# Kernel optimization log

Measured on AMD Instinct MI355X. Metric: run time of the kernel, lower is better.

## Reference

```python
import jax, jax.numpy as jnp
import numpy as np

N_NODES = 50000


def gcn_norm(edge_index, edge_weight, n):
    """PyG GCNConv normalization: add self-loops (weight 1), sym-normalize."""
    src, dst = edge_index[0], edge_index[1]
    loop = jnp.arange(n, dtype=src.dtype)
    src = jnp.concatenate([src, loop])
    dst = jnp.concatenate([dst, loop])
    w = jnp.concatenate([edge_weight, jnp.ones((n,), dtype=edge_weight.dtype)])
    deg = jax.ops.segment_sum(w, dst, num_segments=n)  # in-degree w/ self-loops
    dis = jnp.where(deg > 0, jax.lax.rsqrt(deg), 0.0)  # deg^{-1/2}, inf -> 0
    norm = dis[src] * w * dis[dst]                      # [E+N]
    return src, dst, norm


def gcn_conv(x, src, dst, norm, W, b):
    h = x @ W                                            # [N, F_out]
    msg = norm[:, None] * h[src]                         # gather + scale
    out = jax.ops.segment_sum(msg, dst, num_segments=x.shape[0])  # scatter-add
    return out + b


def setup_inputs() -> dict:
    key = jax.random.key(0)
    ks = jax.random.split(key, 10)
    n, e = N_NODES, 800000
    in_dim, hidden, out_dim = 256, 128, 64
    x = jax.random.normal(ks[0], (n, in_dim), dtype=jnp.float32)
    edge_index = jax.random.randint(ks[1], (2, e), 0, n, dtype=jnp.int32)
    edge_weight = jax.random.uniform(ks[2], (e,), dtype=jnp.float32)
    def glorot(k, fi, fo):
        lim = float(np.sqrt(6.0 / (fi + fo)))
        return jax.random.uniform(k, (fi, fo), minval=-lim, maxval=lim, dtype=jnp.float32)
    return {
        "x": x, "edge_index": edge_index, "edge_weight": edge_weight,
        "W1": glorot(ks[3], in_dim, hidden), "b1": jnp.zeros((hidden,), jnp.float32),
        "W2": glorot(ks[4], hidden, hidden), "b2": jnp.zeros((hidden,), jnp.float32),
        "W3": glorot(ks[5], hidden, out_dim), "b3": jnp.zeros((out_dim,), jnp.float32),
    }


def reference(x, edge_index, edge_weight, W1, b1, W2, b2, W3, b3):
    n = x.shape[0]
    src, dst, norm = gcn_norm(edge_index, edge_weight, n)  # cached=True: shared
    h = jax.nn.relu(gcn_conv(x, src, dst, norm, W1, b1))   # dropout: eval mode no-op
    h = jax.nn.relu(gcn_conv(h, src, dst, norm, W2, b2))
    h = gcn_conv(h, src, dst, norm, W3, b3)
    return h
```

## Files before the change

kernel.cpp:

```cpp
#include <hip/hip_runtime.h>
#include <hip/hip_bf16.h>
#include <stdint.h>

#define NODES 50000
#define EDGES 800000

#define EPB 4096
#define NBLK ((EDGES + EPB - 1) / EPB)
#define NBUK ((NODES + 63) / 64)
#define NBUKP 1024
#define CAP 2560

#define NTILE (NODES / 16)

typedef short bf16x8 __attribute__((ext_vector_type(8)));
typedef float f32x4 __attribute__((ext_vector_type(4)));

__device__ __forceinline__ unsigned short f2bf(float f) {
    union { float f; unsigned u; } v; v.f = f;
    unsigned r = v.u + 0x7fff + ((v.u >> 16) & 1);
    return (unsigned short)(r >> 16);
}
__device__ __forceinline__ float bf2f(unsigned short h) {
    union { float f; unsigned u; } v; v.u = ((unsigned)h) << 16;
    return v.f;
}
__device__ __forceinline__ float bflo(unsigned hv) {
    union { float f; unsigned u; } v; v.u = hv << 16;
    return v.f;
}
__device__ __forceinline__ float bfhi(unsigned hv) {
    union { float f; unsigned u; } v; v.u = hv & 0xffff0000u;
    return v.f;
}

__device__ __forceinline__ void wfrag_one(const float* __restrict__ W, unsigned short* Wf,
                                          int idx, int K, int Nn) {
    int NT = Nn >> 4;
    int lane = idx & 63;
    int f = idx >> 6;
    int nt = f % NT;
    int k0 = (f / NT) << 5;
    int n = (nt << 4) + (lane & 15);
    int kk = k0 + ((lane >> 4) << 3);
    unsigned short o[8];
#pragma unroll
    for (int j = 0; j < 8; j++) o[j] = f2bf(W[(kk + j) * Nn + n]);
    ((uint4*)Wf)[idx] = *(uint4*)o;
}

__global__ void k_setup_hist(const int* __restrict__ dst, unsigned* __restrict__ hist,
                             int* __restrict__ cursor,
                             const float* __restrict__ W1, unsigned short* Wf1,
                             const float* __restrict__ W2, unsigned short* Wf2,
                             const float* __restrict__ W3, unsigned short* Wf3) {
    if ((int)blockIdx.x < NBLK) {
        __shared__ unsigned cnt[NBUK];
        int t = threadIdx.x;
        for (int i = t; i < NBUK; i += 256) cnt[i] = 0;
        __syncthreads();
        int base = blockIdx.x * EPB;
#pragma unroll
        for (int i = 0; i < EPB / 256; i++) {
            int e = base + i * 256 + t;
            if (e < EDGES) atomicAdd(&cnt[((unsigned)dst[e]) >> 6], 1u);
        }
        __syncthreads();
        for (int b = t; b < NBUK; b += 256) hist[b * NBLK + blockIdx.x] = cnt[b];
    } else {
        int idx = (blockIdx.x - NBLK) * 256 + threadIdx.x;
        if (idx == 0) *cursor = 0;
        if (idx < 4096) wfrag_one(W1, Wf1, idx, 256, 128);
        else if (idx < 6144) wfrag_one(W2, Wf2, idx - 4096, 128, 128);
        else if (idx < 7168) wfrag_one(W3, Wf3, idx - 6144, 128, 64);
    }
}

__global__ void k_hscan(unsigned* __restrict__ hist, int2* __restrict__ brange,
                        int* __restrict__ cursor) {
    __shared__ int sm[256];
    __shared__ int s_base;
    int b = blockIdx.x, t = threadIdx.x;
    int v = (t < NBLK) ? (int)hist[b * NBLK + t] : 0;
    sm[t] = v;
    __syncthreads();
    for (int off = 1; off < 256; off <<= 1) {
        int x2 = (t >= off) ? sm[t - off] : 0;
        __syncthreads();
        sm[t] += x2;
        __syncthreads();
    }
    int total = sm[255];
    if (t == 0) s_base = atomicAdd(cursor, total);
    __syncthreads();
    if (t < NBLK) hist[b * NBLK + t] = (unsigned)(s_base + sm[t] - v);
    if (t == 0) { int2 r; r.x = s_base; r.y = total; brange[b] = r; }
}

template <int K, int Nn, bool A_F32>
__device__ __forceinline__ void gemm_tile(const void* __restrict__ A_,
                                          const uint4* __restrict__ Wf,
                                          unsigned short* __restrict__ Hout, int tile) {
    constexpr int NT = Nn / 16;
    int lane = threadIdx.x & 63;
    if (tile * 16 >= NODES) return;
    int row = tile * 16 + (lane & 15);
    int kbase = (lane >> 4) * 8;

    f32x4 acc[NT];
#pragma unroll
    for (int i = 0; i < NT; i++) acc[i] = (f32x4){0.f, 0.f, 0.f, 0.f};

    for (int k0 = 0; k0 < K; k0 += 32) {
        bf16x8 a;
        if (A_F32) {
            const float* A = (const float*)A_;
            const float4* pp = (const float4*)&A[(size_t)row * K + k0 + kbase];
            float4 u0 = pp[0], u1 = pp[1];
            unsigned short t[8];
            t[0] = f2bf(u0.x); t[1] = f2bf(u0.y); t[2] = f2bf(u0.z); t[3] = f2bf(u0.w);
            t[4] = f2bf(u1.x); t[5] = f2bf(u1.y); t[6] = f2bf(u1.z); t[7] = f2bf(u1.w);
            a = *(bf16x8*)t;
        } else {
            const unsigned short* A = (const unsigned short*)A_;
            a = *(const bf16x8*)&A[(size_t)row * K + k0 + kbase];
        }
        int fbase = (k0 >> 5) * NT;
#pragma unroll
        for (int nt = 0; nt < NT; nt++) {
            uint4 braw = Wf[(fbase + nt) * 64 + lane];
            bf16x8 b = *(bf16x8*)&braw;
            acc[nt] = __builtin_amdgcn_mfma_f32_16x16x32_bf16(b, a, acc[nt], 0, 0, 0);
        }
    }
    int xr = lane & 15;
    int wg = lane >> 4;
#pragma unroll
    for (int nt = 0; nt < NT; nt++) {
        uint2 pk;
        pk.x = (unsigned)f2bf(acc[nt][0]) | ((unsigned)f2bf(acc[nt][1]) << 16);
        pk.y = (unsigned)f2bf(acc[nt][2]) | ((unsigned)f2bf(acc[nt][3]) << 16);
        ((uint2*)Hout)[(((size_t)(tile * 16 + xr) * Nn + nt * 16) >> 2) + wg] = pk;
    }
}

__global__ __launch_bounds__(1024) void
k_sort_gemm1(const int* __restrict__ src, const int* __restrict__ dst,
             const float* __restrict__ w, const unsigned* __restrict__ gbase,
             int2* __restrict__ rec,
             const float* __restrict__ x, const uint4* __restrict__ Wf1,
             unsigned short* __restrict__ h) {
    __shared__ unsigned long long rec_lds[EPB];
    __shared__ unsigned cnt[NBUKP];
    __shared__ unsigned lst[NBUKP];
    __shared__ unsigned gb[NBUK];
    __shared__ int sm[1024];

    int blk = blockIdx.x;
    int t = threadIdx.x;
    if (blk & 1) {
        gemm_tile<256, 128, true>((const void*)x, Wf1, h, (blk >> 1) * 16 + (t >> 6));
        return;
    }
    int sb = blk >> 1;
    if (t < NBUK) gb[t] = gbase[t * NBLK + sb];
    cnt[t] = 0;
    __syncthreads();

    int base = sb * EPB;
    int nrec = EDGES - base; if (nrec > EPB) nrec = EPB;

#pragma unroll
    for (int i = 0; i < EPB / 1024; i++) {
        int e = base + i * 1024 + t;
        if (e < EDGES) atomicAdd(&cnt[((unsigned)dst[e]) >> 6], 1u);
    }
    __syncthreads();

    int v = (int)cnt[t];
    sm[t] = v;
    __syncthreads();
    for (int off = 1; off < 1024; off <<= 1) {
        int x2 = (t >= off) ? sm[t - off] : 0;
        __syncthreads();
        sm[t] += x2;
        __syncthreads();
    }
    lst[t] = (unsigned)(sm[t] - v);
    cnt[t] = 0;
    __syncthreads();

#pragma unroll
    for (int i = 0; i < EPB / 1024; i++) {
        int e = base + i * 1024 + t;
        if (e < EDGES) {
            unsigned d = (unsigned)dst[e];
            unsigned b = d >> 6;
            unsigned r = atomicAdd(&cnt[b], 1u);
            unsigned meta = (unsigned)src[e] | ((d & 63u) << 16) | (b << 22);
            rec_lds[lst[b] + r] = (unsigned long long)meta |
                                  ((unsigned long long)__float_as_uint(w[e]) << 32);
        }
    }
    __syncthreads();

    for (int i = t; i < nrec; i += 1024) {
        unsigned long long vv = rec_lds[i];
        unsigned meta = (unsigned)vv;
        unsigned b = meta >> 22;
        unsigned gpos = gb[b] + ((unsigned)i - lst[b]);
        int2 rc; rc.x = (int)(meta & 0x3FFFFFu); rc.y = (int)(vv >> 32);
        rec[gpos] = rc;
    }
}

__global__ void k_sub(int2* __restrict__ rec, const int2* __restrict__ brange,
                      float* __restrict__ dis, int2* __restrict__ rsc) {
    __shared__ int2 stage[CAP];
    __shared__ unsigned short ipos[CAP];
    __shared__ unsigned cnt[64];
    __shared__ unsigned lst[64];
    __shared__ float degw[64];
    int t = threadIdx.x, b = blockIdx.x;
    int2 br = brange[b];
    int base = br.x;
    int n = br.y; if (n > CAP) n = CAP;

    if (t < 64) { cnt[t] = 0; degw[t] = 0.f; }
    __syncthreads();
    for (int i = t; i < n; i += 256) {
        int2 rc = rec[base + i];
        stage[i] = rc;
        unsigned dl = ((unsigned)rc.x >> 16) & 63u;
        atomicAdd(&cnt[dl], 1u);
        atomicAdd(&degw[dl], __int_as_float(rc.y));
    }
    __syncthreads();
    if (t == 0) {
        unsigned run = 0;
        for (int j = 0; j < 64; j++) { lst[j] = run; run += cnt[j]; }
    }
    __syncthreads();
    if (t < 64) {
        int node = b * 64 + t;
        if (node < NODES) {
            dis[node] = rsqrtf(1.0f + degw[t]);
            int2 rs; rs.x = base + (int)lst[t]; rs.y = (int)cnt[t];
            rsc[node] = rs;
        }
    }
    if (t < 64) cnt[t] = 0;
    __syncthreads();
    for (int i = t; i < n; i += 256) {
        unsigned dl = ((unsigned)stage[i].x >> 16) & 63u;
        unsigned r = atomicAdd(&cnt[dl], 1u);
        ipos[lst[dl] + r] = (unsigned short)i;
    }
    __syncthreads();
    for (int i = t; i < n; i += 256) {
        rec[base + i] = stage[ipos[i]];
    }
}

template <int K, int Nn, bool A_F32>
__global__ void k_gemm(const void* __restrict__ A_, const uint4* __restrict__ Wf,
                       unsigned short* __restrict__ Hout) {
    gemm_tile<K, Nn, A_F32>(A_, Wf, Hout, blockIdx.x * 4 + (threadIdx.x >> 6));
}

template <int F, bool RELU, bool OUT_F32>
__global__ void k_agg(const unsigned short* __restrict__ H, const int2* __restrict__ rec,
                      const int2* __restrict__ rsc, const float* __restrict__ dis,
                      const float* __restrict__ bias, void* __restrict__ out_) {
    constexpr int VPT = F / 64;
    int lane = threadIdx.x & 63;
    int node = blockIdx.x * 4 + (threadIdx.x >> 6);
    if (node >= NODES) return;
    node = __builtin_amdgcn_readfirstlane(node);

    const unsigned* H32 = (const unsigned*)H;

    float dn = dis[node];
    float acc0, acc1 = 0.f;
    if (VPT == 2) {
        unsigned hv = H32[node * 64 + lane];
        acc0 = dn * bflo(hv);
        acc1 = dn * bfhi(hv);
    } else {
        acc0 = dn * bf2f(H[node * 64 + lane]);
    }

    int2 rs = rsc[node];
    int beg = rs.x, end = rs.x + rs.y;
    int last = end - 1;
    for (int j = beg; j < end; j += 8) {
        int ss[8]; float nn[8];
#pragma unroll
        for (int q = 0; q < 8; q++) {
            int idx = j + q;
            idx = (idx < last) ? idx : last;
            int2 rc = rec[idx];
            ss[q] = rc.x & 0xFFFF;
            nn[q] = (j + q < end) ? __int_as_float(rc.y) : 0.0f;
        }
#pragma unroll
        for (int q = 0; q < 8; q++) nn[q] *= dis[ss[q]];
        if (VPT == 2) {
            unsigned hh[8];
#pragma unroll
            for (int q = 0; q < 8; q++) hh[q] = H32[ss[q] * 64 + lane];
#pragma unroll
            for (int q = 0; q < 8; q++) {
                acc0 += nn[q] * bflo(hh[q]);
                acc1 += nn[q] * bfhi(hh[q]);
            }
        } else {
            unsigned short hh[8];
#pragma unroll
            for (int q = 0; q < 8; q++) hh[q] = H[ss[q] * 64 + lane];
#pragma unroll
            for (int q = 0; q < 8; q++) acc0 += nn[q] * bf2f(hh[q]);
        }
    }

    if (OUT_F32) {
        float* out = (float*)out_;
        if (VPT == 2) {
            float x0 = dn * acc0 + bias[lane * 2];
            float x1 = dn * acc1 + bias[lane * 2 + 1];
            if (RELU) { x0 = fmaxf(x0, 0.f); x1 = fmaxf(x1, 0.f); }
            out[(size_t)node * F + lane * 2] = x0;
            out[(size_t)node * F + lane * 2 + 1] = x1;
        } else {
            float x0 = dn * acc0 + bias[lane];
            if (RELU) x0 = fmaxf(x0, 0.f);
            out[(size_t)node * F + lane] = x0;
        }
    } else {
        unsigned short* out = (unsigned short*)out_;
        if (VPT == 2) {
            float x0 = dn * acc0 + bias[lane * 2];
            float x1 = dn * acc1 + bias[lane * 2 + 1];
            if (RELU) { x0 = fmaxf(x0, 0.f); x1 = fmaxf(x1, 0.f); }
            unsigned pk = (unsigned)f2bf(x0) | ((unsigned)f2bf(x1) << 16);
            *(unsigned*)&out[(size_t)node * F + lane * 2] = pk;
        } else {
            float x0 = dn * acc0 + bias[lane];
            if (RELU) x0 = fmaxf(x0, 0.f);
            out[(size_t)node * F + lane] = f2bf(x0);
        }
    }
}


extern "C" void kernel_launch(void* const* d_in, const int* in_sizes, int n_in,
                              void* d_out, int out_size, void* d_ws, size_t ws_size,
                              hipStream_t stream) {
    const float* x  = (const float*)d_in[0];
    const int*   ei = (const int*)d_in[1];
    const float* w  = (const float*)d_in[2];
    const float* W1 = (const float*)d_in[3];
    const float* b1 = (const float*)d_in[4];
    const float* W2 = (const float*)d_in[5];
    const float* b2 = (const float*)d_in[6];
    const float* W3 = (const float*)d_in[7];
    const float* b3 = (const float*)d_in[8];
    const int* src = ei;
    const int* dst = ei + EDGES;

    char* p = (char*)d_ws;
    auto alloc = [&](size_t n) { char* r = p; p += (n + 511) & ~(size_t)511; return r; };
    unsigned*       hist   = (unsigned*)alloc((size_t)NBUK * NBLK * 4);
    int2*           brange = (int2*)alloc((size_t)NBUK * 8);
    int*            cursor = (int*)alloc(4);
    int2*           rec    = (int2*)alloc((size_t)EDGES * 8);
    float*          dis    = (float*)alloc(NODES * 4);
    int2*           rsc    = (int2*)alloc((size_t)NODES * 8);
    unsigned short* h      = (unsigned short*)alloc((size_t)NODES * 128 * 2);
    unsigned short* xb     = (unsigned short*)alloc((size_t)NODES * 128 * 2);
    unsigned short* wf1    = (unsigned short*)alloc(256 * 128 * 2);
    unsigned short* wf2    = (unsigned short*)alloc(128 * 128 * 2);
    unsigned short* wf3    = (unsigned short*)alloc(128 * 64 * 2);

    const int TB = 256;

    hipLaunchKernelGGL(k_setup_hist, dim3(NBLK + 28), dim3(TB), 0, stream,
                       dst, hist, cursor, W1, wf1, W2, wf2, W3, wf3);
    hipLaunchKernelGGL(k_hscan, dim3(NBUK), dim3(TB), 0, stream, hist, brange, cursor);
    hipLaunchKernelGGL(k_sort_gemm1, dim3(2 * NBLK), dim3(1024), 0, stream,
                       src, dst, w, hist, rec, x, (const uint4*)wf1, h);
    hipLaunchKernelGGL(k_sub, dim3(NBUK), dim3(TB), 0, stream, rec, brange, dis, rsc);

    int nb_gemm = (NTILE + 3) / 4;
    int nb_agg  = (NODES + 3) / 4;

    hipLaunchKernelGGL((k_agg<128, true, false>), dim3(nb_agg), dim3(TB), 0, stream, h, rec, rsc, dis, b1, (void*)xb);

    hipLaunchKernelGGL((k_gemm<128, 128, false>), dim3(nb_gemm), dim3(TB), 0, stream, (const void*)xb, (const uint4*)wf2, h);
    hipLaunchKernelGGL((k_agg<128, true, false>), dim3(nb_agg), dim3(TB), 0, stream, h, rec, rsc, dis, b2, (void*)xb);

    hipLaunchKernelGGL((k_gemm<128, 64, false>), dim3(nb_gemm), dim3(TB), 0, stream, (const void*)xb, (const uint4*)wf3, h);
    hipLaunchKernelGGL((k_agg<64, false, true>), dim3(nb_agg), dim3(TB), 0, stream, h, rec, rsc, dis, b3, d_out);
}
```

Measured before the change: 305.7 us.

## Split sort from layer-1 GEMM and reuse scanned histogram counts in sort

```diff
diff --git a/kernel.cpp b/kernel.cpp
--- a/kernel.cpp
+++ b/kernel.cpp
@@ -76,8 +76,8 @@
     }
 }
 
-__global__ void k_hscan(unsigned* __restrict__ hist, int2* __restrict__ brange,
-                        int* __restrict__ cursor) {
+__global__ void k_hscan(const unsigned* __restrict__ hist, uint2* __restrict__ cbB,
+                        int2* __restrict__ brange, int* __restrict__ cursor) {
     __shared__ int sm[256];
     __shared__ int s_base;
     int b = blockIdx.x, t = threadIdx.x;
@@ -93,8 +93,128 @@
     int total = sm[255];
     if (t == 0) s_base = atomicAdd(cursor, total);
     __syncthreads();
-    if (t < NBLK) hist[b * NBLK + t] = (unsigned)(s_base + sm[t] - v);
+    if (t < NBLK) {
+        uint2 cb; cb.x = (unsigned)v; cb.y = (unsigned)(s_base + sm[t] - v);
+        cbB[(size_t)t * NBUKP + b] = cb;
+    }
     if (t == 0) { int2 r; r.x = s_base; r.y = total; brange[b] = r; }
+}
+
+__global__ __launch_bounds__(1024) void
+k_sort(const int* __restrict__ src, const int* __restrict__ dst,
+       const float* __restrict__ w, const uint2* __restrict__ cbB,
+       int2* __restrict__ rec) {
+    __shared__ unsigned long long rec_lds[EPB];
+    __shared__ unsigned cnt[NBUKP];
+    __shared__ unsigned lst[NBUKP];
+    __shared__ unsigned gb[NBUKP];
+    __shared__ int wsum[16];
+
+    int sb = blockIdx.x;
+    int t = threadIdx.x;
+    int lane = t & 63;
+    int wid = t >> 6;
+
+    uint2 cb = cbB[(size_t)sb * NBUKP + t];
+    int v = (t < NBUK) ? (int)cb.x : 0;
+    gb[t] = (t < NBUK) ? cb.y : 0u;
+
+    int incl = v;
+#pragma unroll
+    for (int d = 1; d < 64; d <<= 1) {
+        int y = __shfl_up(incl, d, 64);
+        if (lane >= d) incl += y;
+    }
+    if (lane == 63) wsum[wid] = incl;
+    __syncthreads();
+    if (wid == 0) {
+        int s = (lane < 16) ? wsum[lane] : 0;
+#pragma unroll
+        for (int d = 1; d < 16; d <<= 1) {
+            int y = __shfl_up(s, d, 16);
+            if ((lane & 15) >= d) s += y;
+        }
+        if (lane < 16) wsum[lane] = s;
+    }
+    cnt[t] = 0;
+    __syncthreads();
+    int wpre = (wid > 0) ? wsum[wid - 1] : 0;
+    lst[t] = (unsigned)(wpre + incl - v);
+    __syncthreads();
+
+    int base = sb * EPB;
+    int nrec = EDGES - base; if (nrec > EPB) nrec = EPB;
+
+#pragma unroll
+    for (int i = 0; i < EPB / 1024; i++) {
+        int e = base + i * 1024 + t;
+        if (e < EDGES) {
+            unsigned d = (unsigned)dst[e];
+            unsigned b = d >> 6;
+            unsigned r = atomicAdd(&cnt[b], 1u);
+            unsigned meta = (unsigned)src[e] | ((d & 63u) << 16) | (b << 22);
+            rec_lds[lst[b] + r] = (unsigned long long)meta |
+                                  ((unsigned long long)__float_as_uint(w[e]) << 32);
+        }
+    }
+    __syncthreads();
+
+    for (int i = t; i < nrec; i += 1024) {
+        unsigned long long vv = rec_lds[i];
+        unsigned meta = (unsigned)vv;
+        unsigned b = meta >> 22;
+        unsigned gpos = gb[b] + ((unsigned)i - lst[b]);
+        int2 rc; rc.x = (int)(meta & 0x3FFFFFu); rc.y = (int)(vv >> 32);
+        rec[gpos] = rc;
+    }
+}
+
+__global__ void k_sub(int2* __restrict__ rec, const int2* __restrict__ brange,
+                      float* __restrict__ dis, int2* __restrict__ rsc) {
+    __shared__ int2 stage[CAP];
+    __shared__ unsigned short ipos[CAP];
+    __shared__ unsigned cnt[64];
+    __shared__ unsigned lst[64];
+    __shared__ float degw[64];
+    int t = threadIdx.x, b = blockIdx.x;
+    int2 br = brange[b];
+    int base = br.x;
+    int n = br.y; if (n > CAP) n = CAP;
+
+    if (t < 64) { cnt[t] = 0; degw[t] = 0.f; }
+    __syncthreads();
+    for (int i = t; i < n; i += 256) {
+        int2 rc = rec[base + i];
+        stage[i] = rc;
+        unsigned dl = ((unsigned)rc.x >> 16) & 63u;
+        atomicAdd(&cnt[dl], 1u);
+        atomicAdd(&degw[dl], __int_as_float(rc.y));
+    }
+    __syncthreads();
+    if (t == 0) {
+        unsigned run = 0;
+        for (int j = 0; j < 64; j++) { lst[j] = run; run += cnt[j]; }
+    }
+    __syncthreads();
+    if (t < 64) {
+        int node = b * 64 + t;
+        if (node < NODES) {
+            dis[node] = rsqrtf(1.0f + degw[t]);
+            int2 rs; rs.x = base + (int)lst[t]; rs.y = (int)cnt[t];
+            rsc[node] = rs;
+        }
+    }
+    if (t < 64) cnt[t] = 0;
+    __syncthreads();
+    for (int i = t; i < n; i += 256) {
+        unsigned dl = ((unsigned)stage[i].x >> 16) & 63u;
+        unsigned r = atomicAdd(&cnt[dl], 1u);
+        ipos[lst[dl] + r] = (unsigned short)i;
+    }
+    __syncthreads();
+    for (int i = t; i < n; i += 256) {
+        rec[base + i] = stage[ipos[i]];
+    }
 }
 
 template <int K, int Nn, bool A_F32>
@@ -141,124 +261,6 @@
         pk.x = (unsigned)f2bf(acc[nt][0]) | ((unsigned)f2bf(acc[nt][1]) << 16);
         pk.y = (unsigned)f2bf(acc[nt][2]) | ((unsigned)f2bf(acc[nt][3]) << 16);
         ((uint2*)Hout)[(((size_t)(tile * 16 + xr) * Nn + nt * 16) >> 2) + wg] = pk;
-    }
-}
-
-__global__ __launch_bounds__(1024) void
-k_sort_gemm1(const int* __restrict__ src, const int* __restrict__ dst,
-             const float* __restrict__ w, const unsigned* __restrict__ gbase,
-             int2* __restrict__ rec,
-             const float* __restrict__ x, const uint4* __restrict__ Wf1,
-             unsigned short* __restrict__ h) {
-    __shared__ unsigned long long rec_lds[EPB];
-    __shared__ unsigned cnt[NBUKP];
-    __shared__ unsigned lst[NBUKP];
-    __shared__ unsigned gb[NBUK];
-    __shared__ int sm[1024];
-
-    int blk = blockIdx.x;
-    int t = threadIdx.x;
-    if (blk & 1) {
-        gemm_tile<256, 128, true>((const void*)x, Wf1, h, (blk >> 1) * 16 + (t >> 6));
-        return;
-    }
-    int sb = blk >> 1;
-    if (t < NBUK) gb[t] = gbase[t * NBLK + sb];
-    cnt[t] = 0;
-    __syncthreads();
-
-    int base = sb * EPB;
-    int nrec = EDGES - base; if (nrec > EPB) nrec = EPB;
-
-#pragma unroll
-    for (int i = 0; i < EPB / 1024; i++) {
-        int e = base + i * 1024 + t;
-        if (e < EDGES) atomicAdd(&cnt[((unsigned)dst[e]) >> 6], 1u);
-    }
-    __syncthreads();
-
-    int v = (int)cnt[t];
-    sm[t] = v;
-    __syncthreads();
-    for (int off = 1; off < 1024; off <<= 1) {
-        int x2 = (t >= off) ? sm[t - off] : 0;
-        __syncthreads();
-        sm[t] += x2;
-        __syncthreads();
-    }
-    lst[t] = (unsigned)(sm[t] - v);
-    cnt[t] = 0;
-    __syncthreads();
-
-#pragma unroll
-    for (int i = 0; i < EPB / 1024; i++) {
-        int e = base + i * 1024 + t;
-        if (e < EDGES) {
-            unsigned d = (unsigned)dst[e];
-            unsigned b = d >> 6;
-            unsigned r = atomicAdd(&cnt[b], 1u);
-            unsigned meta = (unsigned)src[e] | ((d & 63u) << 16) | (b << 22);
-            rec_lds[lst[b] + r] = (unsigned long long)meta |
-                                  ((unsigned long long)__float_as_uint(w[e]) << 32);
-        }
-    }
-    __syncthreads();
-
-    for (int i = t; i < nrec; i += 1024) {
-        unsigned long long vv = rec_lds[i];
-        unsigned meta = (unsigned)vv;
-        unsigned b = meta >> 22;
-        unsigned gpos = gb[b] + ((unsigned)i - lst[b]);
-        int2 rc; rc.x = (int)(meta & 0x3FFFFFu); rc.y = (int)(vv >> 32);
-        rec[gpos] = rc;
-    }
-}
-
-__global__ void k_sub(int2* __restrict__ rec, const int2* __restrict__ brange,
-                      float* __restrict__ dis, int2* __restrict__ rsc) {
-    __shared__ int2 stage[CAP];
-    __shared__ unsigned short ipos[CAP];
-    __shared__ unsigned cnt[64];
-    __shared__ unsigned lst[64];
-    __shared__ float degw[64];
-    int t = threadIdx.x, b = blockIdx.x;
-    int2 br = brange[b];
-    int base = br.x;
-    int n = br.y; if (n > CAP) n = CAP;
-
-    if (t < 64) { cnt[t] = 0; degw[t] = 0.f; }
-    __syncthreads();
-    for (int i = t; i < n; i += 256) {
-        int2 rc = rec[base + i];
-        stage[i] = rc;
-        unsigned dl = ((unsigned)rc.x >> 16) & 63u;
-        atomicAdd(&cnt[dl], 1u);
-        atomicAdd(&degw[dl], __int_as_float(rc.y));
-    }
-    __syncthreads();
-    if (t == 0) {
-        unsigned run = 0;
-        for (int j = 0; j < 64; j++) { lst[j] = run; run += cnt[j]; }
-    }
-    __syncthreads();
-    if (t < 64) {
-        int node = b * 64 + t;
-        if (node < NODES) {
-            dis[node] = rsqrtf(1.0f + degw[t]);
-            int2 rs; rs.x = base + (int)lst[t]; rs.y = (int)cnt[t];
-            rsc[node] = rs;
-        }
-    }
-    if (t < 64) cnt[t] = 0;
-    __syncthreads();
-    for (int i = t; i < n; i += 256) {
-        unsigned dl = ((unsigned)stage[i].x >> 16) & 63u;
-        unsigned r = atomicAdd(&cnt[dl], 1u);
-        ipos[lst[dl] + r] = (unsigned short)i;
-    }
-    __syncthreads();
-    for (int i = t; i < n; i += 256) {
-        rec[base + i] = stage[ipos[i]];
     }
 }
 
@@ -371,6 +373,7 @@
     char* p = (char*)d_ws;
     auto alloc = [&](size_t n) { char* r = p; p += (n + 511) & ~(size_t)511; return r; };
     unsigned*       hist   = (unsigned*)alloc((size_t)NBUK * NBLK * 4);
+    uint2*          cbB    = (uint2*)alloc((size_t)NBLK * NBUKP * 8);
     int2*           brange = (int2*)alloc((size_t)NBUK * 8);
     int*            cursor = (int*)alloc(4);
     int2*           rec    = (int2*)alloc((size_t)EDGES * 8);
@@ -383,17 +386,16 @@
     unsigned short* wf3    = (unsigned short*)alloc(128 * 64 * 2);
 
     const int TB = 256;
+    int nb_gemm = (NTILE + 3) / 4;
+    int nb_agg  = (NODES + 3) / 4;
 
     hipLaunchKernelGGL(k_setup_hist, dim3(NBLK + 28), dim3(TB), 0, stream,
                        dst, hist, cursor, W1, wf1, W2, wf2, W3, wf3);
-    hipLaunchKernelGGL(k_hscan, dim3(NBUK), dim3(TB), 0, stream, hist, brange, cursor);
-    hipLaunchKernelGGL(k_sort_gemm1, dim3(2 * NBLK), dim3(1024), 0, stream,
-                       src, dst, w, hist, rec, x, (const uint4*)wf1, h);
+    hipLaunchKernelGGL(k_hscan, dim3(NBUK), dim3(TB), 0, stream, hist, cbB, brange, cursor);
+    hipLaunchKernelGGL(k_sort, dim3(NBLK), dim3(1024), 0, stream, src, dst, w, cbB, rec);
     hipLaunchKernelGGL(k_sub, dim3(NBUK), dim3(TB), 0, stream, rec, brange, dis, rsc);
 
-    int nb_gemm = (NTILE + 3) / 4;
-    int nb_agg  = (NODES + 3) / 4;
-
+    hipLaunchKernelGGL((k_gemm<256, 128, true>), dim3(nb_gemm), dim3(TB), 0, stream, (const void*)x, (const uint4*)wf1, h);
     hipLaunchKernelGGL((k_agg<128, true, false>), dim3(nb_agg), dim3(TB), 0, stream, h, rec, rsc, dis, b1, (void*)xb);
 
     hipLaunchKernelGGL((k_gemm<128, 128, false>), dim3(nb_gemm), dim3(TB), 0, stream, (const void*)xb, (const uint4*)wf2, h);
```

After: 296.8 us. 1.03x faster.
